# Kernel optimization log

Measured on AMD Instinct MI355X. Metric: run time of the kernel, lower is better.

Reference implementation:

```python
import jax, jax.numpy as jnp
import numpy as np
from jax import lax

NEG_INF = -1e30

def _binarize(w):
    # BinaryConnect / XNOR-style sign binarization with straight-through estimator
    return w + lax.stop_gradient(jnp.sign(w) - w)

def _conv(x, w, b):
    y = lax.conv_general_dilated(x, w, window_strides=(1, 1), padding='VALID',
                                 dimension_numbers=('NCHW', 'OIHW', 'NCHW'))
    return y + b[None, :, None, None]

def _bn(x, eps, gamma=None, beta=None):
    # training-mode batch norm over (N, H, W)
    mean = jnp.mean(x, axis=(0, 2, 3), keepdims=True)
    var = jnp.var(x, axis=(0, 2, 3), keepdims=True)
    xn = (x - mean) * lax.rsqrt(var + eps)
    if gamma is not None:
        g = jnp.clip(gamma, 0.01, None)  # torch forward clamps BN weight to >=0.01
        xn = xn * g[None, :, None, None] + beta[None, :, None, None]
    return xn

def _maxpool2(x):
    return lax.reduce_window(x, NEG_INF, lax.max, (1, 1, 2, 2), (1, 1, 2, 2), 'VALID')


def setup_inputs() -> dict:
    key = jax.random.key(0)
    ks = jax.random.split(key, 12)
    f = jnp.float32
    return {
        'x': jax.random.normal(ks[0], (8192, 1, 32, 32), dtype=f),
        'conv1_w': jax.random.normal(ks[1], (6, 1, 5, 5), dtype=f) * 0.2,
        'conv1_b': jnp.zeros((6,), dtype=f),
        'conv2_w': jax.random.normal(ks[2], (16, 6, 5, 5), dtype=f) * 0.1,
        'conv2_b': jnp.zeros((16,), dtype=f),
        'bn2_g': jnp.ones((16,), dtype=f),
        'bn2_b': jnp.zeros((16,), dtype=f),
        'conv3_w': jax.random.normal(ks[3], (120, 16, 5, 5), dtype=f) * 0.05,
        'conv3_b': jnp.zeros((120,), dtype=f),
        'bn3_g': jnp.ones((120,), dtype=f),
        'bn3_b': jnp.zeros((120,), dtype=f),
        'fc1_w': jax.random.normal(ks[4], (84, 120), dtype=f) * 0.09,
        'fc1_b': jnp.zeros((84,), dtype=f),
        'fc2_w': jax.random.normal(ks[5], (10, 84), dtype=f) * 0.1,
        'fc2_b': jnp.zeros((10,), dtype=f),
    }


def reference(x, conv1_w, conv1_b, conv2_w, conv2_b, bn2_g, bn2_b,
              conv3_w, conv3_b, bn3_g, bn3_b, fc1_w, fc1_b, fc2_w, fc2_b):
    # layer1: fp conv -> BN(no affine, eps=1e-4) -> relu -> maxpool  [B,6,14,14]
    h = _maxpool2(jax.nn.relu(_bn(_conv(x, conv1_w, conv1_b), 1e-4)))
    # layer2: binary conv -> BN(affine, eps=1e-4) -> relu -> maxpool [B,16,5,5]
    h = _maxpool2(jax.nn.relu(_bn(_conv(h, _binarize(conv2_w), conv2_b), 1e-4, bn2_g, bn2_b)))
    # layer3: binary conv -> BN(affine, eps=1e-5) -> relu            [B,120,1,1]
    h = jax.nn.relu(_bn(_conv(h, _binarize(conv3_w), conv3_b), 1e-5, bn3_g, bn3_b))
    # layer4: binary linear -> relu -> linear                        [B,10]
    h = h.reshape(h.shape[0], -1)  # [B,120]
    h = jax.nn.relu(h @ _binarize(fc1_w).T + fc1_b)
    return h @ fc2_w.T + fc2_b
```

## Files before the change

kernel.cpp:

```cpp
#include <hip/hip_runtime.h>

#define DEVFN __device__ __forceinline__

DEVFN float sgnf(float x) { return (x > 0.f) ? 1.f : ((x < 0.f) ? -1.f : 0.f); }

DEVFN unsigned short f2bf(float x) {
  unsigned int u = __float_as_uint(x);
  unsigned int r = (u + 0x7fffu + ((u >> 16) & 1u)) >> 16;
  return (unsigned short)r;
}

typedef __attribute__((ext_vector_type(8))) short short8;
typedef __attribute__((ext_vector_type(4))) float f32x4;
typedef __attribute__((ext_vector_type(2))) float f32x2;
typedef __attribute__((ext_vector_type(4))) unsigned int u32x4;

#define SUM1 0
#define SQ1  384
#define SUM2 768
#define SQ2  1792
#define SUM3 2816
#define SQ3  10496
#define DBL_BYTES 145408

#define A1 0
#define C1 8
#define A2 16
#define C2 32
#define A3 48
#define C3 168
#define WFR_OFF  3584
#define WFR2_OFF 54784
#define H1_OFF   69632
#define H2_OFF   (H1_OFF + 8192*1176)
#define Y3_OFF   (H2_OFF + 8192*400)

#define RS 17
#define PLANE 238
#define IMGP 1428

__global__ __launch_bounds__(256, 4) void conv1_prep(
    const float* __restrict__ x, const float* __restrict__ w1,
    const float* __restrict__ b1, float* __restrict__ m1,
    double* __restrict__ sums, const float* __restrict__ w2,
    const float* __restrict__ w3, const float* __restrict__ f1,
    unsigned short* __restrict__ wfr3, unsigned short* __restrict__ wfr,
    unsigned short* __restrict__ wfr2) {
  __shared__ f32x2 simg[4 * 1088];
  __shared__ float swtp[6 * 40];
  __shared__ float red[6], redq[6];
  int tid = threadIdx.x;
  if (blockIdx.x >= 1024) {
    int i = (blockIdx.x - 1024) * 256 + tid;
    if (i < 7680) {
      int j = i & 7;
      int t = i >> 3;
      int l = t & 63;
      int c = t >> 6;
      int ch = l & 15;
      int kp = c * 32 + ((l >> 4) << 3) + j;
      int k = kp >> 1;
      int b = k >> 3, kx = k & 7;
      int ci = b / 5, ky = b - 5 * ci;
      float v = (kx < 5) ? sgnf(w2[(ch * 6 + ci) * 25 + ky * 5 + kx]) : 0.f;
      wfr3[i] = f2bf(v);
    }
    if (i < 102400) {
      int j = i & 7;
      int t = i >> 3;
      int l = t & 63;
      int cc = (t >> 6) % 25;
      int nt = (t >> 6) / 25;
      int ch = nt * 16 + (l & 15);
      int kp = cc * 32 + ((l >> 4) << 3) + j;
      float v = (ch < 120) ? sgnf(w3[ch * 400 + (kp >> 1)]) : 0.f;
      wfr[i] = f2bf(v);
    }
    if (i < 24576) {
      int j = i & 7;
      int t = i >> 3;
      int l = t & 63;
      int cc = (t >> 6) & 7;
      int nt = t >> 9;
      int col = nt * 16 + (l & 15);
      int kp = cc * 32 + ((l >> 4) << 3) + j;
      int k = kp >> 1;
      float v = (col < 84 && k < 120) ? sgnf(f1[col * 120 + k]) : 0.f;
      wfr2[i] = f2bf(v);
    }
    return;
  }
  int img0 = blockIdx.x * 8;
  {
    const float2* xg = (const float2*)(x + (size_t)img0 * 1024);
    for (int i2 = tid; i2 < 4096; i2 += 256) {
      int img = i2 >> 9;
      int j = i2 & 511;
      float2 v = xg[img * 512 + j];
      int p = img >> 1, q = img & 1;
      int row = j >> 4, col = (j & 15) * 2;
      float* d0 = (float*)&simg[p * 1088 + row * 34 + col];
      d0[q] = v.x;
      d0[2 + q] = v.y;
    }
  }
  for (int i = tid; i < 240; i += 256) {
    int ch = i / 40, r = i - ch * 40;
    int ky = r >> 3, kx = r & 7;
    swtp[i] = (kx < 5) ? w1[ch * 25 + ky * 5 + kx] : 0.f;
  }
  if (tid < 6) { red[tid] = 0.f; redq[tid] = 0.f; }
  __syncthreads();

  for (int idx = tid; idx < 672; idx += 256) {
    int ch = idx % 6;
    int t = idx / 6;
    int h = t & 1;
    int t2 = t >> 1;
    int py = t2 % 14;
    int p = t2 / 14;
    float bb = b1[ch];
    f32x2 acc0[14], acc1[14];
#pragma unroll
    for (int o = 0; o < 14; ++o) {
      acc0[o] = (f32x2){bb, bb};
      acc1[o] = (f32x2){bb, bb};
    }
    const f32x2* ibase = &simg[p * 1088 + h * 14];
    const float* wch = &swtp[ch * 40];
#pragma unroll
    for (int d = 0; d < 6; ++d) {
      int row = 2 * py + d;
      f32x2 rb[18];
      const f32x4* rp = (const f32x4*)(ibase + row * 34);
#pragma unroll
      for (int tt = 0; tt < 9; ++tt) {
        f32x4 v = rp[tt];
        rb[2 * tt] = (f32x2){v.x, v.y};
        rb[2 * tt + 1] = (f32x2){v.z, v.w};
      }
      if (d < 5) {
        const float* wrow = wch + d * 8;
        f32x4 w4 = *(const f32x4*)wrow;
        float w5[5] = {w4.x, w4.y, w4.z, w4.w, wrow[4]};
#pragma unroll
        for (int kx = 0; kx < 5; ++kx) {
          f32x2 ws = {w5[kx], w5[kx]};
#pragma unroll
          for (int o = 0; o < 14; ++o)
            acc0[o] = __builtin_elementwise_fma(rb[o + kx], ws, acc0[o]);
        }
      }
      if (d >= 1) {
        const float* wrow = wch + (d - 1) * 8;
        f32x4 w4 = *(const f32x4*)wrow;
        float w5[5] = {w4.x, w4.y, w4.z, w4.w, wrow[4]};
#pragma unroll
        for (int kx = 0; kx < 5; ++kx) {
          f32x2 ws = {w5[kx], w5[kx]};
#pragma unroll
          for (int o = 0; o < 14; ++o)
            acc1[o] = __builtin_elementwise_fma(rb[o + kx], ws, acc1[o]);
        }
      }
    }
    f32x2 sv = {0.f, 0.f}, qv = {0.f, 0.f};
#pragma unroll
    for (int o = 0; o < 14; ++o) {
      f32x2 a0 = acc0[o], a1 = acc1[o];
      sv += a0; sv += a1;
      qv = __builtin_elementwise_fma(a0, a0, qv);
      qv = __builtin_elementwise_fma(a1, a1, qv);
    }
    atomicAdd(&red[ch], sv.x + sv.y);
    atomicAdd(&redq[ch], qv.x + qv.y);
    float* mpA = m1 + (size_t)(img0 + 2 * p) * 1176 + ch * 196 + py * 14 + h * 7;
    float* mpB = mpA + 1176;
#pragma unroll
    for (int j = 0; j < 7; ++j) {
      f32x2 m = __builtin_elementwise_max(
          __builtin_elementwise_max(acc0[2 * j], acc0[2 * j + 1]),
          __builtin_elementwise_max(acc1[2 * j], acc1[2 * j + 1]));
      mpA[j] = m.x;
      mpB[j] = m.y;
    }
  }
  __syncthreads();
  if (tid < 6) {
    int slot = blockIdx.x & 63;
    atomicAdd(&sums[SUM1 + tid * 64 + slot], (double)red[tid]);
    atomicAdd(&sums[SQ1 + tid * 64 + slot], (double)redq[tid]);
  }
}

__global__ __launch_bounds__(256) void finalize_bn(
    const double* __restrict__ sum, const double* __restrict__ sq, int nch,
    double invN, double eps, const float* __restrict__ gamma,
    const float* __restrict__ beta, float* __restrict__ a,
    float* __restrict__ c) {
  int t = blockIdx.x * 256 + threadIdx.x;
  int ch = t >> 6, slot = t & 63;
  if (ch >= nch) return;
  double s = sum[ch * 64 + slot];
  double q = sq[ch * 64 + slot];
#pragma unroll
  for (int off = 32; off > 0; off >>= 1) {
    s += __shfl_down(s, off, 64);
    q += __shfl_down(q, off, 64);
  }
  if (slot == 0) {
    double mean = s * invN;
    double var = q * invN - mean * mean;
    float inv = (float)(1.0 / sqrt(var + eps));
    float g = gamma ? fmaxf(gamma[ch], 0.01f) : 1.f;
    float av = g * inv;
    float cv = (beta ? beta[ch] : 0.f) - (float)mean * av;
    a[ch] = av;
    c[ch] = cv;
  }
}

__global__ __launch_bounds__(256, 4) void conv2_mfma(
    const float* __restrict__ m1, const unsigned short* __restrict__ wfr3,
    const float* __restrict__ b2, const float* __restrict__ scales,
    float* __restrict__ m2, double* __restrict__ sums) {
  __shared__ unsigned int Aim[4 * IMGP];
  __shared__ float sa1[6], sc1[6];
  __shared__ float red[16], redq[16];
  int tid = threadIdx.x;
  int img0 = blockIdx.x * 4;
  if (tid < 6) { sa1[tid] = scales[A1 + tid]; sc1[tid] = scales[C1 + tid]; }
  if (tid < 16) { red[tid] = 0.f; redq[tid] = 0.f; }
  for (int i = tid; i < 1008; i += 256) {
    int c3 = i - (i / 3) * 3;
    int t = i / 3;
    int row = t % 14;
    int t2 = t / 14;
    int ci = t2 % 6, img = t2 / 6;
    Aim[img * IMGP + ci * PLANE + row * RS + 14 + c3] = 0u;
  }
  __syncthreads();
  {
    const float2* mg = (const float2*)(m1 + (size_t)img0 * 1176);
    for (int i2 = tid; i2 < 2352; i2 += 256) {
      int img = i2 / 588;
      int e = (i2 - img * 588) * 2;
      int pl = e / 196;
      int rr = e - pl * 196;
      int row = rr / 14, col = rr - row * 14;
      float a = sa1[pl], c = sc1[pl];
      float2 v = mg[i2];
      float v0 = fmaxf(fmaf(a, v.x, c), 0.f);
      float v1 = fmaxf(fmaf(a, v.y, c), 0.f);
      unsigned int h0 = f2bf(v0);
      unsigned int l0 = f2bf(v0 - __uint_as_float(h0 << 16));
      unsigned int h1 = f2bf(v1);
      unsigned int l1 = f2bf(v1 - __uint_as_float(h1 << 16));
      unsigned int* dst = &Aim[img * IMGP + pl * PLANE + row * RS + col];
      dst[0] = h0 | (l0 << 16);
      dst[1] = h1 | (l1 << 16);
    }
  }
  __syncthreads();

  int lane = tid & 63;
  int wv = tid >> 6;
  const short8* bvec = (const short8*)wfr3;
  short8 bf[15];
#pragma unroll
  for (int c = 0; c < 15; ++c) bf[c] = bvec[c * 64 + lane];
  int ch = lane & 15;
  int ag = lane >> 4;
  int agh = ag >> 1, agl = ag & 1;
  float bb = b2[ch];
  float s0 = 0.f, q0 = 0.f;

  for (int t = wv; t < 25; t += 4) {
    int prd = t * 16 + ch;
    int imr = prd / 100;
    int pos = prd - imr * 100;
    int pb = pos >> 2, q = pos & 3;
    int pyr = pb / 5;
    int py = 2 * pyr + (q >> 1);
    int px = 2 * (pb - pyr * 5) + (q & 1);
    const unsigned int* base = &Aim[imr * IMGP + py * RS + px + agl * 4];
    const unsigned int* bR = base + agh * RS;
    const unsigned int* bW = base + agh * 170;
    f32x4 acc = {0.f, 0.f, 0.f, 0.f};
#pragma unroll
    for (int c = 0; c < 15; ++c) {
      const int b0 = 2 * c;
      const int ci0 = b0 / 5, ky0 = b0 % 5;
      const unsigned int* pc =
          ((ky0 == 4) ? bW : bR) + (ci0 * PLANE + ky0 * RS);
      unsigned int a0 = pc[0], a1 = pc[1], a2 = pc[2], a3 = pc[3];
      union { u32x4 u; short8 s; } ua;
      ua.u = (u32x4){a0, a1, a2, a3};
      acc = __builtin_amdgcn_mfma_f32_16x16x32_bf16(ua.s, bf[c], acc, 0, 0, 0);
    }
    int po = t * 4 + ag;
    int imo = po / 25;
    int pbl = po - imo * 25;
    float v0 = acc[0] + bb, v1 = acc[1] + bb;
    float v2 = acc[2] + bb, v3 = acc[3] + bb;
    s0 += (v0 + v1) + (v2 + v3);
    q0 = fmaf(v0, v0, q0); q0 = fmaf(v1, v1, q0);
    q0 = fmaf(v2, v2, q0); q0 = fmaf(v3, v3, q0);
    float mx = fmaxf(fmaxf(v0, v1), fmaxf(v2, v3));
    m2[(size_t)(img0 + imo) * 400 + ch * 25 + pbl] = mx;
  }
  s0 += __shfl_xor(s0, 16, 64); q0 += __shfl_xor(q0, 16, 64);
  s0 += __shfl_xor(s0, 32, 64); q0 += __shfl_xor(q0, 32, 64);
  if (ag == 0) {
    atomicAdd(&red[ch], s0);
    atomicAdd(&redq[ch], q0);
  }
  __syncthreads();
  if (tid < 16) {
    int slot = blockIdx.x & 63;
    atomicAdd(&sums[SUM2 + tid * 64 + slot], (double)red[tid]);
    atomicAdd(&sums[SQ2 + tid * 64 + slot], (double)redq[tid]);
  }
}

__global__ __launch_bounds__(256) void conv3_mfma(
    const float* __restrict__ m2, const unsigned short* __restrict__ wfr,
    const float* __restrict__ b3, const float* __restrict__ scales,
    float* __restrict__ y3, double* __restrict__ sums) {
  __shared__ unsigned int Alds[16 * 404];
  __shared__ float sa2[16], sc2[16];
  __shared__ float red[128], redq[128];
  int tid = threadIdx.x;
  int img0 = blockIdx.x * 16;
  if (tid < 16) { sa2[tid] = scales[A2 + tid]; sc2[tid] = scales[C2 + tid]; }
  if (tid < 128) { red[tid] = 0.f; redq[tid] = 0.f; }
  __syncthreads();
  for (int i4 = tid; i4 < 1600; i4 += 256) {
    int img = i4 / 100, k4 = i4 - img * 100;
    int k = 4 * k4;
    float4 v = *(const float4*)(m2 + (size_t)(img0 + img) * 400 + k);
    float vv[4] = {v.x, v.y, v.z, v.w};
    unsigned int pk[4];
#pragma unroll
    for (int e = 0; e < 4; ++e) {
      int ch = ((k + e) * 41) >> 10;
      float val = fmaxf(fmaf(sa2[ch], vv[e], sc2[ch]), 0.f);
      unsigned int hb = f2bf(val);
      float vh = __uint_as_float(hb << 16);
      unsigned int lb = f2bf(val - vh);
      pk[e] = hb | (lb << 16);
    }
    unsigned int* dst = &Alds[img * 404 + k];
    dst[0] = pk[0]; dst[1] = pk[1]; dst[2] = pk[2]; dst[3] = pk[3];
  }
  __syncthreads();

  int lane = tid & 63;
  int wv = tid >> 6;
  int nt0 = wv * 2, nt1 = wv * 2 + 1;
  const short8* bvec = (const short8*)wfr;
  int arow = lane & 15;
  int ag = lane >> 4;
  f32x4 acc0 = {0.f, 0.f, 0.f, 0.f}, acc1 = {0.f, 0.f, 0.f, 0.f};
  const unsigned short* abase =
      (const unsigned short*)&Alds[arow * 404 + ag * 4];
#pragma unroll 5
  for (int c = 0; c < 25; ++c) {
    short8 af = *(const short8*)(abase + c * 32);
    short8 b0 = bvec[(nt0 * 25 + c) * 64 + lane];
    short8 b1 = bvec[(nt1 * 25 + c) * 64 + lane];
    acc0 = __builtin_amdgcn_mfma_f32_16x16x32_bf16(af, b0, acc0, 0, 0, 0);
    acc1 = __builtin_amdgcn_mfma_f32_16x16x32_bf16(af, b1, acc1, 0, 0, 0);
  }
  int chA = nt0 * 16 + (lane & 15);
  int chB = nt1 * 16 + (lane & 15);
  int rbase = img0 + ((lane >> 4) << 2);
  {
    float bias = b3[chA];
    float s = 0.f, q = 0.f;
#pragma unroll
    for (int r = 0; r < 4; ++r) {
      float v = acc0[r] + bias;
      y3[(size_t)(rbase + r) * 120 + chA] = v;
      s += v; q = fmaf(v, v, q);
    }
    atomicAdd(&red[chA], s);
    atomicAdd(&redq[chA], q);
  }
  if (chB < 120) {
    float bias = b3[chB];
    float s = 0.f, q = 0.f;
#pragma unroll
    for (int r = 0; r < 4; ++r) {
      float v = acc1[r] + bias;
      y3[(size_t)(rbase + r) * 120 + chB] = v;
      s += v; q = fmaf(v, v, q);
    }
    atomicAdd(&red[chB], s);
    atomicAdd(&redq[chB], q);
  }
  __syncthreads();
  if (tid < 120) {
    int slot = blockIdx.x & 63;
    atomicAdd(&sums[SUM3 + tid * 64 + slot], (double)red[tid]);
    atomicAdd(&sums[SQ3 + tid * 64 + slot], (double)redq[tid]);
  }
}

__global__ __launch_bounds__(192) void fc_mfma(
    const float* __restrict__ y3, const float* __restrict__ scales,
    const unsigned short* __restrict__ wfr2, const float* __restrict__ b1,
    const float* __restrict__ w2, const float* __restrict__ b2,
    float* __restrict__ out) {
  __shared__ unsigned int Alds[16 * 132];
  __shared__ float sh4[16 * 88];
  __shared__ float sw2[10 * 85];
  __shared__ float sa3[120], sc3[120];
  __shared__ float sb1[84], sb2[10];
  int tid = threadIdx.x;
  int img0 = blockIdx.x * 16;
  if (tid < 120) { sa3[tid] = scales[A3 + tid]; sc3[tid] = scales[C3 + tid]; }
  if (tid < 84) sb1[tid] = b1[tid];
  if (tid >= 84 && tid < 94) sb2[tid - 84] = b2[tid - 84];
  for (int i = tid; i < 850; i += 192) {
    int o = i / 85, k = i - o * 85;
    sw2[i] = (k < 84) ? w2[o * 84 + k] : 0.f;
  }
  __syncthreads();
  for (int i4 = tid; i4 < 512; i4 += 192) {
    int img = i4 >> 5, k4 = i4 & 31;
    int k = 4 * k4;
    unsigned int pk[4] = {0u, 0u, 0u, 0u};
    if (k4 < 30) {
      float4 v = *(const float4*)(y3 + (size_t)(img0 + img) * 120 + k);
      float vv[4] = {v.x, v.y, v.z, v.w};
#pragma unroll
      for (int e = 0; e < 4; ++e) {
        float val = fmaxf(fmaf(sa3[k + e], vv[e], sc3[k + e]), 0.f);
        unsigned int hb = f2bf(val);
        float vh = __uint_as_float(hb << 16);
        unsigned int lb = f2bf(val - vh);
        pk[e] = hb | (lb << 16);
      }
    }
    unsigned int* dst = &Alds[img * 132 + k];
    dst[0] = pk[0]; dst[1] = pk[1]; dst[2] = pk[2]; dst[3] = pk[3];
  }
  __syncthreads();

  int lane = tid & 63;
  int wv = tid >> 6;
  int nt0 = wv * 2, nt1 = wv * 2 + 1;
  const short8* bvec = (const short8*)wfr2;
  int arow = lane & 15;
  int ag = lane >> 4;
  f32x4 acc0 = {0.f, 0.f, 0.f, 0.f}, acc1 = {0.f, 0.f, 0.f, 0.f};
  const unsigned short* abase =
      (const unsigned short*)&Alds[arow * 132 + ag * 4];
#pragma unroll
  for (int c = 0; c < 8; ++c) {
    short8 af = *(const short8*)(abase + c * 32);
    short8 b0 = bvec[(nt0 * 8 + c) * 64 + lane];
    short8 b1 = bvec[(nt1 * 8 + c) * 64 + lane];
    acc0 = __builtin_amdgcn_mfma_f32_16x16x32_bf16(af, b0, acc0, 0, 0, 0);
    acc1 = __builtin_amdgcn_mfma_f32_16x16x32_bf16(af, b1, acc1, 0, 0, 0);
  }
  {
    int jA = nt0 * 16 + (lane & 15);
    int jB = nt1 * 16 + (lane & 15);
    int r0 = (lane >> 4) << 2;
#pragma unroll
    for (int r = 0; r < 4; ++r)
      sh4[(r0 + r) * 88 + jA] = fmaxf(acc0[r] + sb1[jA], 0.f);
    if (jB < 84) {
#pragma unroll
      for (int r = 0; r < 4; ++r)
        sh4[(r0 + r) * 88 + jB] = fmaxf(acc1[r] + sb1[jB], 0.f);
    }
  }
  __syncthreads();
  if (tid < 160) {
    int img = tid / 10, o = tid - (tid / 10) * 10;
    float acc = sb2[o];
    const float* hp = &sh4[img * 88];
    const float* wp = &sw2[o * 85];
#pragma unroll 4
    for (int k = 0; k < 84; ++k) acc = fmaf(hp[k], wp[k], acc);
    out[(size_t)(img0 + img) * 10 + o] = acc;
  }
}

extern "C" void kernel_launch(void* const* d_in, const int* in_sizes, int n_in,
                              void* d_out, int out_size, void* d_ws,
                              size_t ws_size, hipStream_t stream) {
  const float* x = (const float*)d_in[0];
  const float* conv1_w = (const float*)d_in[1];
  const float* conv1_b = (const float*)d_in[2];
  const float* conv2_w = (const float*)d_in[3];
  const float* conv2_b = (const float*)d_in[4];
  const float* bn2_g = (const float*)d_in[5];
  const float* bn2_b = (const float*)d_in[6];
  const float* conv3_w = (const float*)d_in[7];
  const float* conv3_b = (const float*)d_in[8];
  const float* bn3_g = (const float*)d_in[9];
  const float* bn3_b = (const float*)d_in[10];
  const float* fc1_w = (const float*)d_in[11];
  const float* fc1_b = (const float*)d_in[12];
  const float* fc2_w = (const float*)d_in[13];
  const float* fc2_b = (const float*)d_in[14];
  float* out = (float*)d_out;

  double* sums = (double*)d_ws;
  float* fbase = (float*)((char*)d_ws + DBL_BYTES);
  float* scales = fbase;
  unsigned short* wfr = (unsigned short*)(fbase + WFR_OFF);
  unsigned short* wfr2 = (unsigned short*)(fbase + WFR2_OFF);
  float* m1 = fbase + H1_OFF;
  float* m2 = fbase + H2_OFF;
  float* y3 = fbase + Y3_OFF;
  unsigned short* wfr3 = (unsigned short*)y3;

  hipMemsetAsync(d_ws, 0, DBL_BYTES, stream);

  conv1_prep<<<1424, 256, 0, stream>>>(x, conv1_w, conv1_b, m1, sums, conv2_w,
                                       conv3_w, fc1_w, wfr3, wfr, wfr2);
  finalize_bn<<<2, 256, 0, stream>>>(sums + SUM1, sums + SQ1, 6,
                                     1.0 / (8192.0 * 784.0), 1e-4, nullptr,
                                     nullptr, scales + A1, scales + C1);

  conv2_mfma<<<2048, 256, 0, stream>>>(m1, wfr3, conv2_b, scales, m2, sums);
  finalize_bn<<<4, 256, 0, stream>>>(sums + SUM2, sums + SQ2, 16,
                                     1.0 / (8192.0 * 100.0), 1e-4, bn2_g, bn2_b,
                                     scales + A2, scales + C2);

  conv3_mfma<<<512, 256, 0, stream>>>(m2, wfr, conv3_b, scales, y3, sums);
  finalize_bn<<<30, 256, 0, stream>>>(sums + SUM3, sums + SQ3, 120,
                                      1.0 / 8192.0, 1e-5, bn3_g, bn3_b,
                                      scales + A3, scales + C3);

  fc_mfma<<<512, 192, 0, stream>>>(y3, scales, wfr2, fc1_b, fc2_w, fc2_b, out);
}
```

Baseline: 190.3 us.

## Fuse BN finalize into consumer kernels and duplicate conv2 LDS image for aligned loads

Removes the three finalize_bn launches; each consumer kernel now reduces the 64-slot double partial sums itself to build its BN scale and shift. conv2 also keeps two LDS copies of the input image, an even-aligned one and one shifted by a column, so A-fragment loads can be done as 8-byte vector reads instead of scalar reads. This saves launch gaps and LDS load instructions. In exchange, every block repeats the small reduction, LDS use roughly doubles, and the occupancy hint drops from 4 to 3.

```diff
diff --git a/kernel.cpp b/kernel.cpp
--- a/kernel.cpp
+++ b/kernel.cpp
@@ -14,6 +14,7 @@
 typedef __attribute__((ext_vector_type(4))) float f32x4;
 typedef __attribute__((ext_vector_type(2))) float f32x2;
 typedef __attribute__((ext_vector_type(4))) unsigned int u32x4;
+typedef __attribute__((ext_vector_type(2))) unsigned int u32x2;
 
 #define SUM1 0
 #define SQ1  384
@@ -23,21 +24,15 @@
 #define SQ3  10496
 #define DBL_BYTES 145408
 
-#define A1 0
-#define C1 8
-#define A2 16
-#define C2 32
-#define A3 48
-#define C3 168
 #define WFR_OFF  3584
 #define WFR2_OFF 54784
 #define H1_OFF   69632
 #define H2_OFF   (H1_OFF + 8192*1176)
 #define Y3_OFF   (H2_OFF + 8192*400)
 
-#define RS 17
-#define PLANE 238
-#define IMGP 1428
+#define RS2 18
+#define PLANE2 252
+#define IMGP2 1512
 
 __global__ __launch_bounds__(256, 4) void conv1_prep(
     const float* __restrict__ x, const float* __restrict__ w1,
@@ -193,51 +188,38 @@
   }
 }
 
-__global__ __launch_bounds__(256) void finalize_bn(
-    const double* __restrict__ sum, const double* __restrict__ sq, int nch,
-    double invN, double eps, const float* __restrict__ gamma,
-    const float* __restrict__ beta, float* __restrict__ a,
-    float* __restrict__ c) {
-  int t = blockIdx.x * 256 + threadIdx.x;
-  int ch = t >> 6, slot = t & 63;
-  if (ch >= nch) return;
-  double s = sum[ch * 64 + slot];
-  double q = sq[ch * 64 + slot];
-#pragma unroll
-  for (int off = 32; off > 0; off >>= 1) {
-    s += __shfl_down(s, off, 64);
-    q += __shfl_down(q, off, 64);
-  }
-  if (slot == 0) {
-    double mean = s * invN;
-    double var = q * invN - mean * mean;
-    float inv = (float)(1.0 / sqrt(var + eps));
-    float g = gamma ? fmaxf(gamma[ch], 0.01f) : 1.f;
-    float av = g * inv;
-    float cv = (beta ? beta[ch] : 0.f) - (float)mean * av;
-    a[ch] = av;
-    c[ch] = cv;
-  }
-}
-
-__global__ __launch_bounds__(256, 4) void conv2_mfma(
+__global__ __launch_bounds__(256, 3) void conv2_mfma(
     const float* __restrict__ m1, const unsigned short* __restrict__ wfr3,
-    const float* __restrict__ b2, const float* __restrict__ scales,
-    float* __restrict__ m2, double* __restrict__ sums) {
-  __shared__ unsigned int Aim[4 * IMGP];
+    const float* __restrict__ b2, double* __restrict__ sums,
+    float* __restrict__ m2) {
+  __shared__ unsigned int AimE[4 * IMGP2];
+  __shared__ unsigned int AimS[4 * IMGP2];
   __shared__ float sa1[6], sc1[6];
   __shared__ float red[16], redq[16];
   int tid = threadIdx.x;
   int img0 = blockIdx.x * 4;
-  if (tid < 6) { sa1[tid] = scales[A1 + tid]; sc1[tid] = scales[C1 + tid]; }
+  if (tid < 6) {
+    const double* ps = sums + SUM1 + tid * 64;
+    const double* pq = sums + SQ1 + tid * 64;
+    double s = 0.0, q = 0.0;
+#pragma unroll 8
+    for (int i = 0; i < 64; ++i) { s += ps[i]; q += pq[i]; }
+    double mean = s * (1.0 / (8192.0 * 784.0));
+    double var = q * (1.0 / (8192.0 * 784.0)) - mean * mean;
+    float inv = (float)(1.0 / sqrt(var + 1e-4));
+    sa1[tid] = inv;
+    sc1[tid] = -(float)mean * inv;
+  }
   if (tid < 16) { red[tid] = 0.f; redq[tid] = 0.f; }
-  for (int i = tid; i < 1008; i += 256) {
-    int c3 = i - (i / 3) * 3;
-    int t = i / 3;
-    int row = t % 14;
-    int t2 = t / 14;
+  for (int i = tid; i < 3024; i += 256) {
+    int c9 = i % 9;
+    int rrow = i / 9;
+    int row = rrow % 14;
+    int t2 = rrow / 14;
     int ci = t2 % 6, img = t2 / 6;
-    Aim[img * IMGP + ci * PLANE + row * RS + 14 + c3] = 0u;
+    int base = img * IMGP2 + ci * PLANE2 + row * RS2;
+    if (c9 < 4) AimE[base + 14 + c9] = 0u;
+    else AimS[base + 13 + (c9 - 4)] = 0u;
   }
   __syncthreads();
   {
@@ -256,9 +238,13 @@
       unsigned int l0 = f2bf(v0 - __uint_as_float(h0 << 16));
       unsigned int h1 = f2bf(v1);
       unsigned int l1 = f2bf(v1 - __uint_as_float(h1 << 16));
-      unsigned int* dst = &Aim[img * IMGP + pl * PLANE + row * RS + col];
-      dst[0] = h0 | (l0 << 16);
-      dst[1] = h1 | (l1 << 16);
+      unsigned int p0 = h0 | (l0 << 16);
+      unsigned int p1 = h1 | (l1 << 16);
+      int bidx = img * IMGP2 + pl * PLANE2 + row * RS2 + col;
+      AimE[bidx] = p0;
+      AimE[bidx + 1] = p1;
+      AimS[bidx] = p1;
+      if (col > 0) AimS[bidx - 1] = p0;
     }
   }
   __syncthreads();
@@ -283,19 +269,22 @@
     int pyr = pb / 5;
     int py = 2 * pyr + (q >> 1);
     int px = 2 * (pb - pyr * 5) + (q & 1);
-    const unsigned int* base = &Aim[imr * IMGP + py * RS + px + agl * 4];
-    const unsigned int* bR = base + agh * RS;
-    const unsigned int* bW = base + agh * 170;
+    int par = px & 1;
+    const unsigned int* arr = par ? AimS : AimE;
+    const unsigned int* base =
+        arr + imr * IMGP2 + py * RS2 + (px - par) + agl * 4;
+    const unsigned int* bR = base + agh * RS2;
+    const unsigned int* bW = base + agh * 180;
     f32x4 acc = {0.f, 0.f, 0.f, 0.f};
 #pragma unroll
     for (int c = 0; c < 15; ++c) {
       const int b0 = 2 * c;
       const int ci0 = b0 / 5, ky0 = b0 % 5;
-      const unsigned int* pc =
-          ((ky0 == 4) ? bW : bR) + (ci0 * PLANE + ky0 * RS);
-      unsigned int a0 = pc[0], a1 = pc[1], a2 = pc[2], a3 = pc[3];
+      const u32x2* pc = (const u32x2*)(((ky0 == 4) ? bW : bR) +
+                                       (ci0 * PLANE2 + ky0 * RS2));
+      u32x2 lo = pc[0], hi = pc[1];
       union { u32x4 u; short8 s; } ua;
-      ua.u = (u32x4){a0, a1, a2, a3};
+      ua.u = (u32x4){lo.x, lo.y, hi.x, hi.y};
       acc = __builtin_amdgcn_mfma_f32_16x16x32_bf16(ua.s, bf[c], acc, 0, 0, 0);
     }
     int po = t * 4 + ag;
@@ -325,14 +314,28 @@
 
 __global__ __launch_bounds__(256) void conv3_mfma(
     const float* __restrict__ m2, const unsigned short* __restrict__ wfr,
-    const float* __restrict__ b3, const float* __restrict__ scales,
-    float* __restrict__ y3, double* __restrict__ sums) {
+    const float* __restrict__ b3, const float* __restrict__ bn2_g,
+    const float* __restrict__ bn2_b, double* __restrict__ sums,
+    float* __restrict__ y3) {
   __shared__ unsigned int Alds[16 * 404];
   __shared__ float sa2[16], sc2[16];
   __shared__ float red[128], redq[128];
   int tid = threadIdx.x;
   int img0 = blockIdx.x * 16;
-  if (tid < 16) { sa2[tid] = scales[A2 + tid]; sc2[tid] = scales[C2 + tid]; }
+  if (tid < 16) {
+    const double* ps = sums + SUM2 + tid * 64;
+    const double* pq = sums + SQ2 + tid * 64;
+    double s = 0.0, q = 0.0;
+#pragma unroll 8
+    for (int i = 0; i < 64; ++i) { s += ps[i]; q += pq[i]; }
+    double mean = s * (1.0 / (8192.0 * 100.0));
+    double var = q * (1.0 / (8192.0 * 100.0)) - mean * mean;
+    float inv = (float)(1.0 / sqrt(var + 1e-4));
+    float g = fmaxf(bn2_g[tid], 0.01f);
+    float av = g * inv;
+    sa2[tid] = av;
+    sc2[tid] = bn2_b[tid] - (float)mean * av;
+  }
   if (tid < 128) { red[tid] = 0.f; redq[tid] = 0.f; }
   __syncthreads();
   for (int i4 = tid; i4 < 1600; i4 += 256) {
@@ -408,7 +411,8 @@
 }
 
 __global__ __launch_bounds__(192) void fc_mfma(
-    const float* __restrict__ y3, const float* __restrict__ scales,
+    const float* __restrict__ y3, const double* __restrict__ sums,
+    const float* __restrict__ bn3_g, const float* __restrict__ bn3_b,
     const unsigned short* __restrict__ wfr2, const float* __restrict__ b1,
     const float* __restrict__ w2, const float* __restrict__ b2,
     float* __restrict__ out) {
@@ -419,7 +423,20 @@
   __shared__ float sb1[84], sb2[10];
   int tid = threadIdx.x;
   int img0 = blockIdx.x * 16;
-  if (tid < 120) { sa3[tid] = scales[A3 + tid]; sc3[tid] = scales[C3 + tid]; }
+  if (tid < 120) {
+    const double* ps = sums + SUM3 + tid * 64;
+    const double* pq = sums + SQ3 + tid * 64;
+    double s = 0.0, q = 0.0;
+#pragma unroll 8
+    for (int i = 0; i < 64; ++i) { s += ps[i]; q += pq[i]; }
+    double mean = s * (1.0 / 8192.0);
+    double var = q * (1.0 / 8192.0) - mean * mean;
+    float inv = (float)(1.0 / sqrt(var + 1e-5));
+    float g = fmaxf(bn3_g[tid], 0.01f);
+    float av = g * inv;
+    sa3[tid] = av;
+    sc3[tid] = bn3_b[tid] - (float)mean * av;
+  }
   if (tid < 84) sb1[tid] = b1[tid];
   if (tid >= 84 && tid < 94) sb2[tid - 84] = b2[tid - 84];
   for (int i = tid; i < 850; i += 192) {
@@ -512,7 +529,6 @@
 
   double* sums = (double*)d_ws;
   float* fbase = (float*)((char*)d_ws + DBL_BYTES);
-  float* scales = fbase;
   unsigned short* wfr = (unsigned short*)(fbase + WFR_OFF);
   unsigned short* wfr2 = (unsigned short*)(fbase + WFR2_OFF);
   float* m1 = fbase + H1_OFF;
@@ -524,19 +540,9 @@
 
   conv1_prep<<<1424, 256, 0, stream>>>(x, conv1_w, conv1_b, m1, sums, conv2_w,
                                        conv3_w, fc1_w, wfr3, wfr, wfr2);
-  finalize_bn<<<2, 256, 0, stream>>>(sums + SUM1, sums + SQ1, 6,
-                                     1.0 / (8192.0 * 784.0), 1e-4, nullptr,
-                                     nullptr, scales + A1, scales + C1);
-
-  conv2_mfma<<<2048, 256, 0, stream>>>(m1, wfr3, conv2_b, scales, m2, sums);
-  finalize_bn<<<4, 256, 0, stream>>>(sums + SUM2, sums + SQ2, 16,
-                                     1.0 / (8192.0 * 100.0), 1e-4, bn2_g, bn2_b,
-                                     scales + A2, scales + C2);
-
-  conv3_mfma<<<512, 256, 0, stream>>>(m2, wfr, conv3_b, scales, y3, sums);
-  finalize_bn<<<30, 256, 0, stream>>>(sums + SUM3, sums + SQ3, 120,
-                                      1.0 / 8192.0, 1e-5, bn3_g, bn3_b,
-                                      scales + A3, scales + C3);
-
-  fc_mfma<<<512, 192, 0, stream>>>(y3, scales, wfr2, fc1_b, fc2_w, fc2_b, out);
+  conv2_mfma<<<2048, 256, 0, stream>>>(m1, wfr3, conv2_b, sums, m2);
+  conv3_mfma<<<512, 256, 0, stream>>>(m2, wfr, conv3_b, bn2_g, bn2_b, sums,
+                                      y3);
+  fc_mfma<<<512, 192, 0, stream>>>(y3, sums, bn3_g, bn3_b, wfr2, fc1_b, fc2_w,
+                                   fc2_b, out);
 }
```

New measurement: 225.9 us. 18.8% more time.

## Fuse BN finalize into producer kernels via last-block atomic counter

Applied to the files above, without the earlier changes.

Removes the three separate finalize_bn launches. Each conv kernel now increments a global block counter after pushing its partial sums, and the last block to finish reduces the statistics and writes the BN scale/shift. This cuts kernel launch gaps and small-kernel tail latency. In exchange every block pays a threadfence plus an atomic, and the serial finalize runs on a single block at the end of each kernel.

```diff
diff --git a/kernel.cpp b/kernel.cpp
--- a/kernel.cpp
+++ b/kernel.cpp
@@ -21,7 +21,9 @@
 #define SQ2  1792
 #define SUM3 2816
 #define SQ3  10496
+#define CNT_OFF 18176
 #define DBL_BYTES 145408
+#define ZERO_BYTES 145472
 
 #define A1 0
 #define C1 8
@@ -39,16 +41,44 @@
 #define PLANE 238
 #define IMGP 1428
 
+DEVFN void finalize_layer(const double* __restrict__ sum,
+                          const double* __restrict__ sq, int nch, double invN,
+                          double eps, const float* __restrict__ gamma,
+                          const float* __restrict__ beta,
+                          float* __restrict__ a, float* __restrict__ c,
+                          int tid) {
+  int lane = tid & 63, wv = tid >> 6;
+  for (int ch = wv; ch < nch; ch += 4) {
+    double s = sum[ch * 64 + lane];
+    double q = sq[ch * 64 + lane];
+#pragma unroll
+    for (int off = 32; off > 0; off >>= 1) {
+      s += __shfl_down(s, off, 64);
+      q += __shfl_down(q, off, 64);
+    }
+    if (lane == 0) {
+      double mean = s * invN;
+      double var = q * invN - mean * mean;
+      float inv = (float)(1.0 / sqrt(var + eps));
+      float g = gamma ? fmaxf(gamma[ch], 0.01f) : 1.f;
+      float av = g * inv;
+      a[ch] = av;
+      c[ch] = (beta ? beta[ch] : 0.f) - (float)mean * av;
+    }
+  }
+}
+
 __global__ __launch_bounds__(256, 4) void conv1_prep(
     const float* __restrict__ x, const float* __restrict__ w1,
     const float* __restrict__ b1, float* __restrict__ m1,
     double* __restrict__ sums, const float* __restrict__ w2,
     const float* __restrict__ w3, const float* __restrict__ f1,
     unsigned short* __restrict__ wfr3, unsigned short* __restrict__ wfr,
-    unsigned short* __restrict__ wfr2) {
+    unsigned short* __restrict__ wfr2, float* __restrict__ scales) {
   __shared__ f32x2 simg[4 * 1088];
   __shared__ float swtp[6 * 40];
   __shared__ float red[6], redq[6];
+  __shared__ int lastF;
   int tid = threadIdx.x;
   if (blockIdx.x >= 1024) {
     int i = (blockIdx.x - 1024) * 256 + tid;
@@ -191,42 +221,30 @@
     atomicAdd(&sums[SUM1 + tid * 64 + slot], (double)red[tid]);
     atomicAdd(&sums[SQ1 + tid * 64 + slot], (double)redq[tid]);
   }
-}
-
-__global__ __launch_bounds__(256) void finalize_bn(
-    const double* __restrict__ sum, const double* __restrict__ sq, int nch,
-    double invN, double eps, const float* __restrict__ gamma,
-    const float* __restrict__ beta, float* __restrict__ a,
-    float* __restrict__ c) {
-  int t = blockIdx.x * 256 + threadIdx.x;
-  int ch = t >> 6, slot = t & 63;
-  if (ch >= nch) return;
-  double s = sum[ch * 64 + slot];
-  double q = sq[ch * 64 + slot];
-#pragma unroll
-  for (int off = 32; off > 0; off >>= 1) {
-    s += __shfl_down(s, off, 64);
-    q += __shfl_down(q, off, 64);
-  }
-  if (slot == 0) {
-    double mean = s * invN;
-    double var = q * invN - mean * mean;
-    float inv = (float)(1.0 / sqrt(var + eps));
-    float g = gamma ? fmaxf(gamma[ch], 0.01f) : 1.f;
-    float av = g * inv;
-    float cv = (beta ? beta[ch] : 0.f) - (float)mean * av;
-    a[ch] = av;
-    c[ch] = cv;
+  __threadfence();
+  __syncthreads();
+  if (tid == 0) {
+    unsigned* cnt = (unsigned*)(sums + CNT_OFF);
+    lastF = (atomicAdd(&cnt[0], 1u) == 1023u);
+  }
+  __syncthreads();
+  if (lastF) {
+    __threadfence();
+    finalize_layer(sums + SUM1, sums + SQ1, 6, 1.0 / (8192.0 * 784.0), 1e-4,
+                   nullptr, nullptr, scales + A1, scales + C1, tid);
   }
 }
 
 __global__ __launch_bounds__(256, 4) void conv2_mfma(
     const float* __restrict__ m1, const unsigned short* __restrict__ wfr3,
     const float* __restrict__ b2, const float* __restrict__ scales,
-    float* __restrict__ m2, double* __restrict__ sums) {
+    float* __restrict__ m2, double* __restrict__ sums,
+    const float* __restrict__ bn2_g, const float* __restrict__ bn2_b,
+    float* __restrict__ scw) {
   __shared__ unsigned int Aim[4 * IMGP];
   __shared__ float sa1[6], sc1[6];
   __shared__ float red[16], redq[16];
+  __shared__ int lastF;
   int tid = threadIdx.x;
   int img0 = blockIdx.x * 4;
   if (tid < 6) { sa1[tid] = scales[A1 + tid]; sc1[tid] = scales[C1 + tid]; }
@@ -321,15 +339,30 @@
     atomicAdd(&sums[SUM2 + tid * 64 + slot], (double)red[tid]);
     atomicAdd(&sums[SQ2 + tid * 64 + slot], (double)redq[tid]);
   }
+  __threadfence();
+  __syncthreads();
+  if (tid == 0) {
+    unsigned* cnt = (unsigned*)(sums + CNT_OFF);
+    lastF = (atomicAdd(&cnt[1], 1u) == 2047u);
+  }
+  __syncthreads();
+  if (lastF) {
+    __threadfence();
+    finalize_layer(sums + SUM2, sums + SQ2, 16, 1.0 / (8192.0 * 100.0), 1e-4,
+                   bn2_g, bn2_b, scw + A2, scw + C2, tid);
+  }
 }
 
 __global__ __launch_bounds__(256) void conv3_mfma(
     const float* __restrict__ m2, const unsigned short* __restrict__ wfr,
     const float* __restrict__ b3, const float* __restrict__ scales,
-    float* __restrict__ y3, double* __restrict__ sums) {
+    float* __restrict__ y3, double* __restrict__ sums,
+    const float* __restrict__ bn3_g, const float* __restrict__ bn3_b,
+    float* __restrict__ scw) {
   __shared__ unsigned int Alds[16 * 404];
   __shared__ float sa2[16], sc2[16];
   __shared__ float red[128], redq[128];
+  __shared__ int lastF;
   int tid = threadIdx.x;
   int img0 = blockIdx.x * 16;
   if (tid < 16) { sa2[tid] = scales[A2 + tid]; sc2[tid] = scales[C2 + tid]; }
@@ -404,6 +437,18 @@
     int slot = blockIdx.x & 63;
     atomicAdd(&sums[SUM3 + tid * 64 + slot], (double)red[tid]);
     atomicAdd(&sums[SQ3 + tid * 64 + slot], (double)redq[tid]);
+  }
+  __threadfence();
+  __syncthreads();
+  if (tid == 0) {
+    unsigned* cnt = (unsigned*)(sums + CNT_OFF);
+    lastF = (atomicAdd(&cnt[2], 1u) == 511u);
+  }
+  __syncthreads();
+  if (lastF) {
+    __threadfence();
+    finalize_layer(sums + SUM3, sums + SQ3, 120, 1.0 / 8192.0, 1e-5, bn3_g,
+                   bn3_b, scw + A3, scw + C3, tid);
   }
 }
 
@@ -511,7 +556,7 @@
   float* out = (float*)d_out;
 
   double* sums = (double*)d_ws;
-  float* fbase = (float*)((char*)d_ws + DBL_BYTES);
+  float* fbase = (float*)((char*)d_ws + ZERO_BYTES);
   float* scales = fbase;
   unsigned short* wfr = (unsigned short*)(fbase + WFR_OFF);
   unsigned short* wfr2 = (unsigned short*)(fbase + WFR2_OFF);
@@ -520,23 +565,14 @@
   float* y3 = fbase + Y3_OFF;
   unsigned short* wfr3 = (unsigned short*)y3;
 
-  hipMemsetAsync(d_ws, 0, DBL_BYTES, stream);
+  hipMemsetAsync(d_ws, 0, ZERO_BYTES, stream);
 
   conv1_prep<<<1424, 256, 0, stream>>>(x, conv1_w, conv1_b, m1, sums, conv2_w,
-                                       conv3_w, fc1_w, wfr3, wfr, wfr2);
-  finalize_bn<<<2, 256, 0, stream>>>(sums + SUM1, sums + SQ1, 6,
-                                     1.0 / (8192.0 * 784.0), 1e-4, nullptr,
-                                     nullptr, scales + A1, scales + C1);
-
-  conv2_mfma<<<2048, 256, 0, stream>>>(m1, wfr3, conv2_b, scales, m2, sums);
-  finalize_bn<<<4, 256, 0, stream>>>(sums + SUM2, sums + SQ2, 16,
-                                     1.0 / (8192.0 * 100.0), 1e-4, bn2_g, bn2_b,
-                                     scales + A2, scales + C2);
-
-  conv3_mfma<<<512, 256, 0, stream>>>(m2, wfr, conv3_b, scales, y3, sums);
-  finalize_bn<<<30, 256, 0, stream>>>(sums + SUM3, sums + SQ3, 120,
-                                      1.0 / 8192.0, 1e-5, bn3_g, bn3_b,
-                                      scales + A3, scales + C3);
-
+                                       conv3_w, fc1_w, wfr3, wfr, wfr2,
+                                       scales);
+  conv2_mfma<<<2048, 256, 0, stream>>>(m1, wfr3, conv2_b, scales, m2, sums,
+                                       bn2_g, bn2_b, scales);
+  conv3_mfma<<<512, 256, 0, stream>>>(m2, wfr, conv3_b, scales, y3, sums,
+                                      bn3_g, bn3_b, scales);
   fc_mfma<<<512, 192, 0, stream>>>(y3, scales, wfr2, fc1_b, fc2_w, fc2_b, out);
 }
```

Result: slower. 620.5 us (+226.1%).
